# Kernel optimization log

Hardware: AMD Instinct MI355X
Metric: run time of the kernel (lower is better)

Reference implementation:

```python
import jax, jax.numpy as jnp
import numpy as np

NEG = -1e9


def setup_inputs() -> dict:
    key = jax.random.key(0)
    ks = jax.random.split(key, 5)
    B, N, D = 2, 1024, 40
    x = jax.random.normal(ks[0], (B, N, D), dtype=jnp.float32)
    # Linear(2D->D): store as (2D, D) so y = cat @ W1 + b1 (transposed torch layout)
    W1 = jax.random.normal(ks[1], (2 * D, D), dtype=jnp.float32) * (1.0 / np.sqrt(2 * D))
    b1 = jax.random.normal(ks[2], (D,), dtype=jnp.float32) * 0.01
    W2 = jax.random.normal(ks[3], (D, D), dtype=jnp.float32) * (1.0 / np.sqrt(D))
    b2 = jax.random.normal(ks[4], (D,), dtype=jnp.float32) * 0.01
    return {"x": x, "W1": W1, "b1": b1, "W2": W2, "b2": b2}


def reference(x, W1, b1, W2, b2):
    B, N, D = x.shape
    # cat([xi, xj]) @ W1 == xi @ W1[:D] + xj @ W1[D:] -> avoid (B,N,N,2D) materialization
    ai = x @ W1[:D]          # (B, N, D), contribution of row index i
    aj = x @ W1[D:]          # (B, N, D), contribution of col index j
    h = jax.nn.gelu(ai[:, :, None, :] + aj[:, None, :, :] + b1, approximate=False)  # (B,N,N,D)
    p = h @ W2 + b2          # (B, N, N, D)
    mask = jnp.triu(jnp.ones((N, N), dtype=bool), 1)  # True where j > i (masked out)
    p = jnp.where(mask[None, :, :, None], 0.0, p)
    sq = jnp.sum(p * p, axis=-1)                       # (B, N, N)
    s = jnp.sqrt(jnp.where(mask[None], 1.0, sq))       # safe sqrt at masked zeros
    s = jnp.where(mask[None], NEG, s)
    w = jax.nn.softmax(s, axis=-1)                     # softmax over j
    return jnp.sum(w[..., None] * p, axis=2)           # (B, N, D)
```

## Files before the change

### kernel.cpp

```cpp
#include <hip/hip_runtime.h>
#include <math.h>

#define D 40
#define NN 1024
#define BB 2

typedef __attribute__((ext_vector_type(8))) _Float16 f16x8;
typedef __attribute__((ext_vector_type(4))) float f32x4;

__device__ __forceinline__ unsigned int pk16(float a, float b) {
    return __builtin_bit_cast(unsigned int, __builtin_amdgcn_cvt_pkrtz(a, b));
}

__device__ __forceinline__ float gelu_tanh(float a) {
    float u = a * a;
    float t1 = fmaf(0.10294366f, u, 2.3022083f);
    float e = __builtin_amdgcn_exp2f(a * t1);
    float r = __builtin_amdgcn_rcpf(e + 1.0f);
    return fmaf(-a, r, a);
}

__device__ __forceinline__ f16x8 frag8(float4 a0, float4 a1, float4 x0, float4 x1) {
    float g0 = gelu_tanh(a0.x + x0.x);
    float g1 = gelu_tanh(a0.y + x0.y);
    float g2 = gelu_tanh(a0.z + x0.z);
    float g3 = gelu_tanh(a0.w + x0.w);
    float g4 = gelu_tanh(a1.x + x1.x);
    float g5 = gelu_tanh(a1.y + x1.y);
    float g6 = gelu_tanh(a1.z + x1.z);
    float g7 = gelu_tanh(a1.w + x1.w);
    return __builtin_bit_cast(f16x8,
        make_uint4(pk16(g0, g1), pk16(g2, g3), pk16(g4, g5), pk16(g6, g7)));
}

__global__ __launch_bounds__(64) void precompute_kernel(
    const float* __restrict__ x, const float* __restrict__ W1,
    const float* __restrict__ b1, const float* __restrict__ W2,
    float* __restrict__ ai, float* __restrict__ aj, uint4* __restrict__ w2fT) {
    int r = blockIdx.x;
    int t = threadIdx.x;
    __shared__ float xr[D];
    if (t < D) xr[t] = x[(size_t)r * D + t];
    __syncthreads();
    if (t < D) {
        float s1 = b1[t];
        float s2 = 0.0f;
#pragma unroll
        for (int k = 0; k < D; ++k) {
            float xv = xr[k];
            s1 = fmaf(xv, W1[k * D + t], s1);
            s2 = fmaf(xv, W1[(D + k) * D + t], s2);
        }
        ai[(size_t)r * D + t] = s1;
        aj[(size_t)r * D + t] = s2;
    }
    if (r == 0) {
        const int lr = t & 15, lg = t >> 4;
#pragma unroll
        for (int mt = 0; mt < 3; ++mt)
#pragma unroll
            for (int kt = 0; kt < 2; ++kt) {
                unsigned int u[4];
#pragma unroll
                for (int pe = 0; pe < 4; ++pe) {
                    int k0 = kt * 32 + lg * 8 + pe * 2;
                    int dd = mt * 16 + lr;
                    float v0 = (k0 < D && dd < D) ? W2[k0 * D + dd] : 0.0f;
                    float v1 = (k0 + 1 < D && dd < D) ? W2[(k0 + 1) * D + dd] : 0.0f;
                    u[pe] = pk16(v0, v1);
                }
                w2fT[(mt * 2 + kt) * 64 + t] = make_uint4(u[0], u[1], u[2], u[3]);
            }
    }
}

__global__ void pair_kernel(
    const float* __restrict__ ai_g, const float* __restrict__ aj_g,
    const uint4* __restrict__ w2fT, const float* __restrict__ b2,
    float* __restrict__ out) {
    __shared__ float mbuf[224];

    const int t = threadIdx.x;
    const int bid = blockIdx.x;
    const int bb = bid & 1;
    const int i = NN - 1 - (bid >> 1);
    const int w = t >> 6;
    const int l = t & 63;
    const int lr = l & 15;
    const int lg = l >> 4;

    f16x8 w2t[3][2];
#pragma unroll
    for (int mt = 0; mt < 3; ++mt)
#pragma unroll
        for (int kt = 0; kt < 2; ++kt)
            w2t[mt][kt] = __builtin_bit_cast(f16x8, w2fT[(mt * 2 + kt) * 64 + l]);

    float bv2[3][4];
#pragma unroll
    for (int mt = 0; mt < 3; ++mt)
#pragma unroll
        for (int r = 0; r < 4; ++r) {
            int d = mt * 16 + lg * 4 + r;
            bv2[mt][r] = (d < D) ? b2[d] : 0.0f;
        }

    const float* air_p = ai_g + ((size_t)bb * NN + i) * D + (lg << 3);
    float4 air[2][2];
    air[0][0] = *reinterpret_cast<const float4*>(air_p);
    air[0][1] = *reinterpret_cast<const float4*>(air_p + 4);
    air[1][0] = *reinterpret_cast<const float4*>(air_p + 32);
    air[1][1] = *reinterpret_cast<const float4*>(air_p + 36);

    const float* aj_b = aj_g + (size_t)bb * NN * D;

    float m_run = 0.0f, l_run = 0.0f;
    float o[3][4];
#pragma unroll
    for (int mt = 0; mt < 3; ++mt)
#pragma unroll
        for (int r = 0; r < 4; ++r) o[mt][r] = 0.0f;

    for (int jbase = w << 5; jbase <= i; jbase += 128) {
        f32x4 acc[3][2];
#pragma unroll
        for (int mt = 0; mt < 3; ++mt)
#pragma unroll
            for (int n = 0; n < 2; ++n)
                acc[mt][n] = (f32x4){0.0f, 0.0f, 0.0f, 0.0f};

#pragma unroll
        for (int n = 0; n < 2; ++n) {
            const int j = jbase + n * 16 + lr;
            const int jsrc = min(j, i);
            const float* ajr = aj_b + (size_t)jsrc * D + (lg << 3);
            float4 q0 = *reinterpret_cast<const float4*>(ajr);
            float4 q1 = *reinterpret_cast<const float4*>(ajr + 4);
            float4 q2 = *reinterpret_cast<const float4*>(ajr + 32);
            float4 q3 = *reinterpret_cast<const float4*>(ajr + 36);
            f16x8 B0 = frag8(air[0][0], air[0][1], q0, q1);
            f16x8 B1 = frag8(air[1][0], air[1][1], q2, q3);
#pragma unroll
            for (int mt = 0; mt < 3; ++mt) {
                acc[mt][n] = __builtin_amdgcn_mfma_f32_16x16x32_f16(
                    w2t[mt][0], B0, acc[mt][n], 0, 0, 0);
                acc[mt][n] = __builtin_amdgcn_mfma_f32_16x16x32_f16(
                    w2t[mt][1], B1, acc[mt][n], 0, 0, 0);
            }
        }

        float sv[2];
#pragma unroll
        for (int n = 0; n < 2; ++n) {
            float sq = 0.0f;
#pragma unroll
            for (int mt = 0; mt < 3; ++mt)
#pragma unroll
                for (int r = 0; r < 4; ++r) {
                    float p = acc[mt][n][r] + bv2[mt][r];
                    acc[mt][n][r] = p;
                    sq = fmaf(p, p, sq);
                }
            sq += __shfl_xor(sq, 16);
            sq += __shfl_xor(sq, 32);
            int j = jbase + n * 16 + lr;
            sv[n] = (j <= i) ? __builtin_amdgcn_sqrtf(sq) : -1e30f;
        }
        float mx = fmaxf(sv[0], sv[1]);
        mx = fmaxf(mx, __shfl_xor(mx, 1));
        mx = fmaxf(mx, __shfl_xor(mx, 2));
        mx = fmaxf(mx, __shfl_xor(mx, 4));
        mx = fmaxf(mx, __shfl_xor(mx, 8));
        if (mx > m_run) {
            float scale = __expf(m_run - mx);
            l_run *= scale;
#pragma unroll
            for (int mt = 0; mt < 3; ++mt)
#pragma unroll
                for (int r = 0; r < 4; ++r) o[mt][r] *= scale;
            m_run = mx;
        }
        float w0 = __expf(sv[0] - m_run);
        float w1 = __expf(sv[1] - m_run);
        l_run += w0 + w1;
#pragma unroll
        for (int mt = 0; mt < 3; ++mt)
#pragma unroll
            for (int r = 0; r < 4; ++r)
                o[mt][r] = fmaf(w0, acc[mt][0][r], fmaf(w1, acc[mt][1][r], o[mt][r]));
    }

#pragma unroll
    for (int mt = 0; mt < 3; ++mt)
#pragma unroll
        for (int r = 0; r < 4; ++r) {
            float v = o[mt][r];
            v += __shfl_xor(v, 1);
            v += __shfl_xor(v, 2);
            v += __shfl_xor(v, 4);
            v += __shfl_xor(v, 8);
            o[mt][r] = v;
        }
    l_run += __shfl_xor(l_run, 1);
    l_run += __shfl_xor(l_run, 2);
    l_run += __shfl_xor(l_run, 4);
    l_run += __shfl_xor(l_run, 8);

    if (lr == 0) {
#pragma unroll
        for (int mt = 0; mt < 3; ++mt)
#pragma unroll
            for (int r = 0; r < 4; ++r) {
                int d = mt * 16 + lg * 4 + r;
                if (d < D) mbuf[w * 56 + d] = o[mt][r];
            }
        if (lg == 0) { mbuf[w * 56 + 48] = l_run; mbuf[w * 56 + 49] = m_run; }
    }
    __syncthreads();
    if (t < D) {
        float M = fmaxf(fmaxf(mbuf[49], mbuf[56 + 49]),
                        fmaxf(mbuf[112 + 49], mbuf[168 + 49]));
        float L = 0.0f, val = 0.0f;
#pragma unroll
        for (int ww = 0; ww < 4; ++ww) {
            float c = __expf(mbuf[ww * 56 + 49] - M);
            L = fmaf(c, mbuf[ww * 56 + 48], L);
            val = fmaf(c, mbuf[ww * 56 + t], val);
        }
        out[((size_t)bb * NN + i) * D + t] = val / L;
    }
}

extern "C" void kernel_launch(void* const* d_in, const int* in_sizes, int n_in,
                              void* d_out, int out_size, void* d_ws, size_t ws_size,
                              hipStream_t stream) {
    const float* x  = (const float*)d_in[0];
    const float* W1 = (const float*)d_in[1];
    const float* b1 = (const float*)d_in[2];
    const float* W2 = (const float*)d_in[3];
    const float* b2 = (const float*)d_in[4];
    float* out = (float*)d_out;

    float* ai = (float*)d_ws;
    float* aj = ai + (size_t)BB * NN * D;
    uint4* w2fT = (uint4*)(aj + (size_t)BB * NN * D);

    precompute_kernel<<<BB * NN, 64, 0, stream>>>(x, W1, b1, W2, ai, aj, w2fT);
    pair_kernel<<<BB * NN, 256, 0, stream>>>(ai, aj, w2fT, b2, out);
}
```

Baseline: 39.26 us.

## Software-pipeline aj row loads and fold b2 into MFMA accumulator init

Splits the per-iteration aj loads so the second half-tile and the next iteration's first half-tile are fetched one step ahead of the GELU/MFMA work that consumes the previous one. The MFMA accumulators start from the b2 bias, which removes the separate bias adds. Loop-invariant values are pinned in VGPRs with empty asm, and occupancy hints are added via launch_bounds and waves_per_eu. The extra live registers for prefetched data raise register pressure, and the prefetch beyond i is clamped by min, so it stays in bounds.

```diff
diff --git a/kernel.cpp b/kernel.cpp
--- a/kernel.cpp
+++ b/kernel.cpp
@@ -18,6 +18,16 @@
     float e = __builtin_amdgcn_exp2f(a * t1);
     float r = __builtin_amdgcn_rcpf(e + 1.0f);
     return fmaf(-a, r, a);
+}
+
+__device__ __forceinline__ void pinf(float& x) { asm volatile("" : "+v"(x)); }
+__device__ __forceinline__ void pin4(float4& v) {
+    asm volatile("" : "+v"(v.x), "+v"(v.y), "+v"(v.z), "+v"(v.w));
+}
+__device__ __forceinline__ void pin8(f16x8& v) {
+    uint4 u = __builtin_bit_cast(uint4, v);
+    asm volatile("" : "+v"(u.x), "+v"(u.y), "+v"(u.z), "+v"(u.w));
+    v = __builtin_bit_cast(f16x8, u);
 }
 
 __device__ __forceinline__ f16x8 frag8(float4 a0, float4 a1, float4 x0, float4 x1) {
@@ -74,7 +84,9 @@
     }
 }
 
-__global__ void pair_kernel(
+__global__ __launch_bounds__(256)
+__attribute__((amdgpu_waves_per_eu(2, 4)))
+void pair_kernel(
     const float* __restrict__ ai_g, const float* __restrict__ aj_g,
     const uint4* __restrict__ w2fT, const float* __restrict__ b2,
     float* __restrict__ out) {
@@ -93,8 +105,10 @@
 #pragma unroll
     for (int mt = 0; mt < 3; ++mt)
 #pragma unroll
-        for (int kt = 0; kt < 2; ++kt)
+        for (int kt = 0; kt < 2; ++kt) {
             w2t[mt][kt] = __builtin_bit_cast(f16x8, w2fT[(mt * 2 + kt) * 64 + l]);
+            pin8(w2t[mt][kt]);
+        }
 
     float bv2[3][4];
 #pragma unroll
@@ -103,14 +117,15 @@
         for (int r = 0; r < 4; ++r) {
             int d = mt * 16 + lg * 4 + r;
             bv2[mt][r] = (d < D) ? b2[d] : 0.0f;
+            pinf(bv2[mt][r]);
         }
 
     const float* air_p = ai_g + ((size_t)bb * NN + i) * D + (lg << 3);
-    float4 air[2][2];
-    air[0][0] = *reinterpret_cast<const float4*>(air_p);
-    air[0][1] = *reinterpret_cast<const float4*>(air_p + 4);
-    air[1][0] = *reinterpret_cast<const float4*>(air_p + 32);
-    air[1][1] = *reinterpret_cast<const float4*>(air_p + 36);
+    float4 air00 = *reinterpret_cast<const float4*>(air_p);
+    float4 air01 = *reinterpret_cast<const float4*>(air_p + 4);
+    float4 air10 = *reinterpret_cast<const float4*>(air_p + 32);
+    float4 air11 = *reinterpret_cast<const float4*>(air_p + 36);
+    pin4(air00); pin4(air01); pin4(air10); pin4(air11);
 
     const float* aj_b = aj_g + (size_t)bb * NN * D;
 
@@ -121,31 +136,49 @@
 #pragma unroll
         for (int r = 0; r < 4; ++r) o[mt][r] = 0.0f;
 
-    for (int jbase = w << 5; jbase <= i; jbase += 128) {
+    float4 qa0, qa1, qa2, qa3, qb0, qb1, qb2, qb3;
+    auto ldq = [&](int jt, float4& d0, float4& d1, float4& d2, float4& d3) {
+        const int jsrc = min(jt + lr, i);
+        const float* ajr = aj_b + (size_t)jsrc * D + (lg << 3);
+        d0 = *reinterpret_cast<const float4*>(ajr);
+        d1 = *reinterpret_cast<const float4*>(ajr + 4);
+        d2 = *reinterpret_cast<const float4*>(ajr + 32);
+        d3 = *reinterpret_cast<const float4*>(ajr + 36);
+    };
+
+    const int jb0 = w << 5;
+    ldq(jb0, qa0, qa1, qa2, qa3);
+
+    for (int jbase = jb0; jbase <= i; jbase += 128) {
         f32x4 acc[3][2];
 #pragma unroll
         for (int mt = 0; mt < 3; ++mt)
 #pragma unroll
             for (int n = 0; n < 2; ++n)
-                acc[mt][n] = (f32x4){0.0f, 0.0f, 0.0f, 0.0f};
-
-#pragma unroll
-        for (int n = 0; n < 2; ++n) {
-            const int j = jbase + n * 16 + lr;
-            const int jsrc = min(j, i);
-            const float* ajr = aj_b + (size_t)jsrc * D + (lg << 3);
-            float4 q0 = *reinterpret_cast<const float4*>(ajr);
-            float4 q1 = *reinterpret_cast<const float4*>(ajr + 4);
-            float4 q2 = *reinterpret_cast<const float4*>(ajr + 32);
-            float4 q3 = *reinterpret_cast<const float4*>(ajr + 36);
-            f16x8 B0 = frag8(air[0][0], air[0][1], q0, q1);
-            f16x8 B1 = frag8(air[1][0], air[1][1], q2, q3);
+                acc[mt][n] = (f32x4){bv2[mt][0], bv2[mt][1], bv2[mt][2], bv2[mt][3]};
+
+        ldq(jbase + 16, qb0, qb1, qb2, qb3);
+        {
+            f16x8 B0 = frag8(air00, air01, qa0, qa1);
+            f16x8 B1 = frag8(air10, air11, qa2, qa3);
 #pragma unroll
             for (int mt = 0; mt < 3; ++mt) {
-                acc[mt][n] = __builtin_amdgcn_mfma_f32_16x16x32_f16(
-                    w2t[mt][0], B0, acc[mt][n], 0, 0, 0);
-                acc[mt][n] = __builtin_amdgcn_mfma_f32_16x16x32_f16(
-                    w2t[mt][1], B1, acc[mt][n], 0, 0, 0);
+                acc[mt][0] = __builtin_amdgcn_mfma_f32_16x16x32_f16(
+                    w2t[mt][0], B0, acc[mt][0], 0, 0, 0);
+                acc[mt][0] = __builtin_amdgcn_mfma_f32_16x16x32_f16(
+                    w2t[mt][1], B1, acc[mt][0], 0, 0, 0);
+            }
+        }
+        ldq(jbase + 128, qa0, qa1, qa2, qa3);
+        {
+            f16x8 B0 = frag8(air00, air01, qb0, qb1);
+            f16x8 B1 = frag8(air10, air11, qb2, qb3);
+#pragma unroll
+            for (int mt = 0; mt < 3; ++mt) {
+                acc[mt][1] = __builtin_amdgcn_mfma_f32_16x16x32_f16(
+                    w2t[mt][0], B0, acc[mt][1], 0, 0, 0);
+                acc[mt][1] = __builtin_amdgcn_mfma_f32_16x16x32_f16(
+                    w2t[mt][1], B1, acc[mt][1], 0, 0, 0);
             }
         }
 
@@ -156,11 +189,8 @@
 #pragma unroll
             for (int mt = 0; mt < 3; ++mt)
 #pragma unroll
-                for (int r = 0; r < 4; ++r) {
-                    float p = acc[mt][n][r] + bv2[mt][r];
-                    acc[mt][n][r] = p;
-                    sq = fmaf(p, p, sq);
-                }
+                for (int r = 0; r < 4; ++r)
+                    sq = fmaf(acc[mt][n][r], acc[mt][n][r], sq);
             sq += __shfl_xor(sq, 16);
             sq += __shfl_xor(sq, 32);
             int j = jbase + n * 16 + lr;
```

After: 42.18 us. 1.07x slower.

## Compute GELU in packed fp16, dedupe tail K-block via bpermute, widen j tile

Applied to the files above, without the earlier changes.

Stores ai/aj in packed fp16 and evaluates GELU with half2 arithmetic, halving the transcendental and ALU work per pair. The second K-block holds only 8 real elements (32..39), so each lane computes GELU for one j and the values are shared across lanes with ds_bpermute instead of being recomputed. Each iteration now covers 64 j values per wave, bias is folded into the accumulator init, the per-iteration max reduction across lanes is replaced by lazy per-lane rescaling with a threshold of 8, and the per-lane max is reconciled once at the end. This trades accuracy (fp16 GELU inputs and exp) and more registers for less VALU work per pair.

```diff
diff --git a/kernel.cpp b/kernel.cpp
--- a/kernel.cpp
+++ b/kernel.cpp
@@ -1,9 +1,11 @@
 #include <hip/hip_runtime.h>
+#include <hip/hip_fp16.h>
 #include <math.h>
 
 #define D 40
 #define NN 1024
 #define BB 2
+#define RH 20
 
 typedef __attribute__((ext_vector_type(8))) _Float16 f16x8;
 typedef __attribute__((ext_vector_type(4))) float f32x4;
@@ -12,34 +14,28 @@
     return __builtin_bit_cast(unsigned int, __builtin_amdgcn_cvt_pkrtz(a, b));
 }
 
-__device__ __forceinline__ float gelu_tanh(float a) {
-    float u = a * a;
-    float t1 = fmaf(0.10294366f, u, 2.3022083f);
-    float e = __builtin_amdgcn_exp2f(a * t1);
-    float r = __builtin_amdgcn_rcpf(e + 1.0f);
-    return fmaf(-a, r, a);
-}
-
-__device__ __forceinline__ f16x8 frag8(float4 a0, float4 a1, float4 x0, float4 x1) {
-    float g0 = gelu_tanh(a0.x + x0.x);
-    float g1 = gelu_tanh(a0.y + x0.y);
-    float g2 = gelu_tanh(a0.z + x0.z);
-    float g3 = gelu_tanh(a0.w + x0.w);
-    float g4 = gelu_tanh(a1.x + x1.x);
-    float g5 = gelu_tanh(a1.y + x1.y);
-    float g6 = gelu_tanh(a1.z + x1.z);
-    float g7 = gelu_tanh(a1.w + x1.w);
-    return __builtin_bit_cast(f16x8,
-        make_uint4(pk16(g0, g1), pk16(g2, g3), pk16(g4, g5), pk16(g6, g7)));
+__device__ __forceinline__ unsigned int gelu2u(unsigned int a_u, unsigned int x_u) {
+    __half2 a = __builtin_bit_cast(__half2, a_u);
+    __half2 x = __builtin_bit_cast(__half2, x_u);
+    __half2 s = __hadd2(a, x);
+    __half2 u = __hmul2(s, s);
+    __half2 t1 = __hfma2(__float2half2_rn(0.10294366f), u,
+                         __float2half2_rn(2.3022083f));
+    __half2 z = __hmul2(s, t1);
+    __half2 e = h2exp2(z);
+    __half2 r = h2rcp(__hadd2(e, __float2half2_rn(1.0f)));
+    __half2 g = __hsub2(s, __hmul2(s, r));
+    return __builtin_bit_cast(unsigned int, g);
 }
 
 __global__ __launch_bounds__(64) void precompute_kernel(
     const float* __restrict__ x, const float* __restrict__ W1,
     const float* __restrict__ b1, const float* __restrict__ W2,
-    float* __restrict__ ai, float* __restrict__ aj, uint4* __restrict__ w2fT) {
+    unsigned int* __restrict__ ai16, unsigned int* __restrict__ aj16,
+    uint4* __restrict__ w2fT) {
     int r = blockIdx.x;
     int t = threadIdx.x;
-    __shared__ float xr[D];
+    __shared__ float xr[D], s1s[D], s2s[D];
     if (t < D) xr[t] = x[(size_t)r * D + t];
     __syncthreads();
     if (t < D) {
@@ -51,8 +47,13 @@
             s1 = fmaf(xv, W1[k * D + t], s1);
             s2 = fmaf(xv, W1[(D + k) * D + t], s2);
         }
-        ai[(size_t)r * D + t] = s1;
-        aj[(size_t)r * D + t] = s2;
+        s1s[t] = s1;
+        s2s[t] = s2;
+    }
+    __syncthreads();
+    if (t < RH) {
+        ai16[(size_t)r * RH + t] = pk16(s1s[2 * t], s1s[2 * t + 1]);
+        aj16[(size_t)r * RH + t] = pk16(s2s[2 * t], s2s[2 * t + 1]);
     }
     if (r == 0) {
         const int lr = t & 15, lg = t >> 4;
@@ -74,8 +75,8 @@
     }
 }
 
-__global__ void pair_kernel(
-    const float* __restrict__ ai_g, const float* __restrict__ aj_g,
+__global__ __launch_bounds__(256) void pair_kernel(
+    const unsigned int* __restrict__ ai16, const unsigned int* __restrict__ aj16,
     const uint4* __restrict__ w2fT, const float* __restrict__ b2,
     float* __restrict__ out) {
     __shared__ float mbuf[224];
@@ -105,14 +106,10 @@
             bv2[mt][r] = (d < D) ? b2[d] : 0.0f;
         }
 
-    const float* air_p = ai_g + ((size_t)bb * NN + i) * D + (lg << 3);
-    float4 air[2][2];
-    air[0][0] = *reinterpret_cast<const float4*>(air_p);
-    air[0][1] = *reinterpret_cast<const float4*>(air_p + 4);
-    air[1][0] = *reinterpret_cast<const float4*>(air_p + 32);
-    air[1][1] = *reinterpret_cast<const float4*>(air_p + 36);
-
-    const float* aj_b = aj_g + (size_t)bb * NN * D;
+    const unsigned int* ai_row = ai16 + ((size_t)bb * NN + i) * RH;
+    const uint4 aiA = *reinterpret_cast<const uint4*>(ai_row + 4 * lg);
+    const uint4 aiT = *reinterpret_cast<const uint4*>(ai_row + 16);
+    const unsigned int* aj_b = aj16 + (size_t)bb * NN * RH;
 
     float m_run = 0.0f, l_run = 0.0f;
     float o[3][4];
@@ -121,57 +118,70 @@
 #pragma unroll
         for (int r = 0; r < 4; ++r) o[mt][r] = 0.0f;
 
-    for (int jbase = w << 5; jbase <= i; jbase += 128) {
-        f32x4 acc[3][2];
-#pragma unroll
-        for (int mt = 0; mt < 3; ++mt)
-#pragma unroll
-            for (int n = 0; n < 2; ++n)
-                acc[mt][n] = (f32x4){0.0f, 0.0f, 0.0f, 0.0f};
-
-#pragma unroll
-        for (int n = 0; n < 2; ++n) {
-            const int j = jbase + n * 16 + lr;
-            const int jsrc = min(j, i);
-            const float* ajr = aj_b + (size_t)jsrc * D + (lg << 3);
-            float4 q0 = *reinterpret_cast<const float4*>(ajr);
-            float4 q1 = *reinterpret_cast<const float4*>(ajr + 4);
-            float4 q2 = *reinterpret_cast<const float4*>(ajr + 32);
-            float4 q3 = *reinterpret_cast<const float4*>(ajr + 36);
-            f16x8 B0 = frag8(air[0][0], air[0][1], q0, q1);
-            f16x8 B1 = frag8(air[1][0], air[1][1], q2, q3);
+    for (int jbase = w << 6; jbase <= i; jbase += 256) {
+        uint4 ajA[4], ajT;
+#pragma unroll
+        for (int n = 0; n < 4; ++n) {
+            const int j0 = min(jbase + n * 16 + lr, i);
+            ajA[n] = *reinterpret_cast<const uint4*>(aj_b + (size_t)j0 * RH + 4 * lg);
+        }
+        {
+            const int jt = min(jbase + l, i);
+            ajT = *reinterpret_cast<const uint4*>(aj_b + (size_t)jt * RH + 16);
+        }
+
+        unsigned int pd0 = gelu2u(aiT.x, ajT.x);
+        unsigned int pd1 = gelu2u(aiT.y, ajT.y);
+        unsigned int pd2 = gelu2u(aiT.z, ajT.z);
+        unsigned int pd3 = gelu2u(aiT.w, ajT.w);
+
+        f32x4 acc[3][4];
+#pragma unroll
+        for (int mt = 0; mt < 3; ++mt)
+#pragma unroll
+            for (int n = 0; n < 4; ++n)
+                acc[mt][n] = (f32x4){bv2[mt][0], bv2[mt][1], bv2[mt][2], bv2[mt][3]};
+
+#pragma unroll
+        for (int n = 0; n < 4; ++n) {
+            uint4 Bu;
+            Bu.x = gelu2u(aiA.x, ajA[n].x);
+            Bu.y = gelu2u(aiA.y, ajA[n].y);
+            Bu.z = gelu2u(aiA.z, ajA[n].z);
+            Bu.w = gelu2u(aiA.w, ajA[n].w);
+            f16x8 B = __builtin_bit_cast(f16x8, Bu);
+            const int idx = (lr << 2) + (n << 6);
+            uint4 Tu;
+            Tu.x = __builtin_amdgcn_ds_bpermute(idx, pd0);
+            Tu.y = __builtin_amdgcn_ds_bpermute(idx, pd1);
+            Tu.z = __builtin_amdgcn_ds_bpermute(idx, pd2);
+            Tu.w = __builtin_amdgcn_ds_bpermute(idx, pd3);
+            f16x8 Bt = __builtin_bit_cast(f16x8, Tu);
 #pragma unroll
             for (int mt = 0; mt < 3; ++mt) {
                 acc[mt][n] = __builtin_amdgcn_mfma_f32_16x16x32_f16(
-                    w2t[mt][0], B0, acc[mt][n], 0, 0, 0);
+                    w2t[mt][0], B, acc[mt][n], 0, 0, 0);
                 acc[mt][n] = __builtin_amdgcn_mfma_f32_16x16x32_f16(
-                    w2t[mt][1], B1, acc[mt][n], 0, 0, 0);
+                    w2t[mt][1], Bt, acc[mt][n], 0, 0, 0);
             }
         }
 
-        float sv[2];
-#pragma unroll
-        for (int n = 0; n < 2; ++n) {
+        float sv[4];
+#pragma unroll
+        for (int n = 0; n < 4; ++n) {
             float sq = 0.0f;
 #pragma unroll
             for (int mt = 0; mt < 3; ++mt)
 #pragma unroll
-                for (int r = 0; r < 4; ++r) {
-                    float p = acc[mt][n][r] + bv2[mt][r];
-                    acc[mt][n][r] = p;
-                    sq = fmaf(p, p, sq);
-                }
+                for (int r = 0; r < 4; ++r)
+                    sq = fmaf(acc[mt][n][r], acc[mt][n][r], sq);
             sq += __shfl_xor(sq, 16);
             sq += __shfl_xor(sq, 32);
             int j = jbase + n * 16 + lr;
             sv[n] = (j <= i) ? __builtin_amdgcn_sqrtf(sq) : -1e30f;
         }
-        float mx = fmaxf(sv[0], sv[1]);
-        mx = fmaxf(mx, __shfl_xor(mx, 1));
-        mx = fmaxf(mx, __shfl_xor(mx, 2));
-        mx = fmaxf(mx, __shfl_xor(mx, 4));
-        mx = fmaxf(mx, __shfl_xor(mx, 8));
-        if (mx > m_run) {
+        float mx = fmaxf(fmaxf(sv[0], sv[1]), fmaxf(sv[2], sv[3]));
+        if (mx > m_run + 8.0f) {
             float scale = __expf(m_run - mx);
             l_run *= scale;
 #pragma unroll
@@ -182,19 +192,31 @@
         }
         float w0 = __expf(sv[0] - m_run);
         float w1 = __expf(sv[1] - m_run);
-        l_run += w0 + w1;
+        float w2 = __expf(sv[2] - m_run);
+        float w3 = __expf(sv[3] - m_run);
+        l_run += (w0 + w1) + (w2 + w3);
 #pragma unroll
         for (int mt = 0; mt < 3; ++mt)
 #pragma unroll
             for (int r = 0; r < 4; ++r)
-                o[mt][r] = fmaf(w0, acc[mt][0][r], fmaf(w1, acc[mt][1][r], o[mt][r]));
-    }
-
+                o[mt][r] = fmaf(w0, acc[mt][0][r],
+                           fmaf(w1, acc[mt][1][r],
+                           fmaf(w2, acc[mt][2][r],
+                           fmaf(w3, acc[mt][3][r], o[mt][r]))));
+    }
+
+    float M = m_run;
+    M = fmaxf(M, __shfl_xor(M, 1));
+    M = fmaxf(M, __shfl_xor(M, 2));
+    M = fmaxf(M, __shfl_xor(M, 4));
+    M = fmaxf(M, __shfl_xor(M, 8));
+    float c0 = __expf(m_run - M);
+    l_run *= c0;
 #pragma unroll
     for (int mt = 0; mt < 3; ++mt)
 #pragma unroll
         for (int r = 0; r < 4; ++r) {
-            float v = o[mt][r];
+            float v = o[mt][r] * c0;
             v += __shfl_xor(v, 1);
             v += __shfl_xor(v, 2);
             v += __shfl_xor(v, 4);
@@ -214,16 +236,16 @@
                 int d = mt * 16 + lg * 4 + r;
                 if (d < D) mbuf[w * 56 + d] = o[mt][r];
             }
-        if (lg == 0) { mbuf[w * 56 + 48] = l_run; mbuf[w * 56 + 49] = m_run; }
+        if (lg == 0) { mbuf[w * 56 + 48] = l_run; mbuf[w * 56 + 49] = M; }
     }
     __syncthreads();
     if (t < D) {
-        float M = fmaxf(fmaxf(mbuf[49], mbuf[56 + 49]),
-                        fmaxf(mbuf[112 + 49], mbuf[168 + 49]));
+        float Mg = fmaxf(fmaxf(mbuf[49], mbuf[56 + 49]),
+                         fmaxf(mbuf[112 + 49], mbuf[168 + 49]));
         float L = 0.0f, val = 0.0f;
 #pragma unroll
         for (int ww = 0; ww < 4; ++ww) {
-            float c = __expf(mbuf[ww * 56 + 49] - M);
+            float c = __expf(mbuf[ww * 56 + 49] - Mg);
             L = fmaf(c, mbuf[ww * 56 + 48], L);
             val = fmaf(c, mbuf[ww * 56 + t], val);
         }
@@ -241,10 +263,10 @@
     const float* b2 = (const float*)d_in[4];
     float* out = (float*)d_out;
 
-    float* ai = (float*)d_ws;
-    float* aj = ai + (size_t)BB * NN * D;
-    uint4* w2fT = (uint4*)(aj + (size_t)BB * NN * D);
-
-    precompute_kernel<<<BB * NN, 64, 0, stream>>>(x, W1, b1, W2, ai, aj, w2fT);
-    pair_kernel<<<BB * NN, 256, 0, stream>>>(ai, aj, w2fT, b2, out);
-}
+    unsigned int* ai16 = (unsigned int*)d_ws;
+    unsigned int* aj16 = ai16 + (size_t)BB * NN * RH;
+    uint4* w2fT = (uint4*)(aj16 + (size_t)BB * NN * RH);
+
+    precompute_kernel<<<BB * NN, 64, 0, stream>>>(x, W1, b1, W2, ai16, aj16, w2fT);
+    pair_kernel<<<BB * NN, 256, 0, stream>>>(ai16, aj16, w2fT, b2, out);
+}
```

New measurement: 38.13 us. -2.9%, faster.
